# Performance work log

Hardware: AMD Instinct MI355X
Metric: run time of the kernel (lower is better)

The kernel has to match this reference:

```python
import jax, jax.numpy as jnp
import numpy as np

B, C, H, W = 32, 512, 28, 28
NC, NM, K = 50, 4, 5          # num_classes, num_mixtures, num_clutter_models
OCC = 0.3                     # occ_likely[0]


def setup_inputs() -> dict:
    key = jax.random.key(0)
    k1, k2, k3 = jax.random.split(key, 3)
    x = jax.random.uniform(k1, (B, C, H, W), dtype=jnp.float32)
    mix_model = jax.random.uniform(k2, (NC * NM, C, H, W), dtype=jnp.float32)
    clutter_model = jax.random.uniform(k3, (K, C), dtype=jnp.float32)
    return {"x": x, "mix_model": mix_model, "clutter_model": clutter_model}


def _l1_normalize(a, axis):
    # torch: F.normalize(torch.clamp(a, 0, 1), p=1, dim=axis) with eps=1e-12
    a = jnp.clip(a, 0.0, 1.0)
    return a / jnp.maximum(jnp.sum(a, axis=axis, keepdims=True), 1e-12)


def reference(x, mix_model, clutter_model):
    # clutter: [K, C] -> L1-normalized over channels
    cl = _l1_normalize(clutter_model, axis=1)
    # background log-likelihood: (x.unsqueeze(1) * cl[:, :, None, None]).sum(2)
    bg = jnp.einsum('bchw,kc->bkhw', x, cl)            # [B, K, H, W]
    bg = jnp.log(bg * OCC + 1e-10)
    # mixture models: [M, C, H, W] -> L1-normalized over channels
    mm = _l1_normalize(mix_model, axis=1)
    # foreground log-likelihood: (x.unsqueeze(1) * mm).sum(2)
    fg = jnp.einsum('bchw,mchw->bmhw', x, mm)          # [B, M, H, W]
    fg = jnp.log(fg * (1.0 - OCC) + 1e-10)
    fg = fg.reshape(B, NC, NM, 1, H, W)
    # per-pixel occlusion max between foreground and background, sum over H, W
    per_model = jnp.maximum(fg, bg[:, None, None, :, :, :]).sum((-1, -2))  # [B, NC, NM, K]
    # max over clutter models, then over mixtures
    return per_model.max(axis=-1).max(axis=-1)          # [B, NC]
```

## Files before the change

kernel.cpp:

```cpp
#include <hip/hip_runtime.h>
#include <math.h>

#define Bc  32
#define Cc  512
#define HWc 784
#define Mc  200
#define Kc  5
#define NCc 50

#define PTm   16
#define MTm   16
#define NMB   13
#define NPB   49
#define CKm   32
#define NCHm  16
#define RSTR  18
#define XPL   (32*RSTR)
#define MPL   (16*RSTR)
#define MMBASE (16*XPL)
#define LDSDW (16*XPL + 16*MPL)

typedef short s8v __attribute__((ext_vector_type(8)));
typedef float f4v __attribute__((ext_vector_type(4)));

union F8 { uint2 u2[2]; s8v h; };

__device__ __forceinline__ unsigned f2b(float f) {
    union { float f; unsigned u; } v; v.f = f;
    return (v.u + 0x7FFFu + ((v.u >> 16) & 1u)) >> 16;
}
__device__ __forceinline__ unsigned pk(float lo, float hi) {
    return f2b(lo) | (f2b(hi) << 16);
}

__global__ __launch_bounds__(256) void k_bg(const float* __restrict__ x,
                                            const float* __restrict__ clut,
                                            float* __restrict__ bgpart) {
    __shared__ float cl[Kc * Cc];
    __shared__ float csum[Kc];
    const int t = threadIdx.x;
    for (int i = t; i < Kc * Cc; i += 256) cl[i] = clut[i];
    __syncthreads();
    if (t < 160) {
        const int k = t >> 5, l = t & 31;
        float s = 0.0f;
        for (int c = l; c < Cc; c += 32) s += cl[k * Cc + c];
#pragma unroll
        for (int off = 16; off > 0; off >>= 1) s += __shfl_down(s, off, 32);
        if (l == 0) csum[k] = fmaxf(s, 1e-12f);
    }
    __syncthreads();

    const int b = blockIdx.x;
    const int z = blockIdx.z;
    const int hw = blockIdx.y * 256 + t;
    if (hw < HWc) {
        float acc[Kc] = {0.f, 0.f, 0.f, 0.f, 0.f};
        const int cbase = z * 128;
        const float* xb = x + ((size_t)b * Cc + cbase) * HWc + hw;
#pragma unroll 4
        for (int c = 0; c < 128; ++c) {
            const float xv = xb[c * HWc];
#pragma unroll
            for (int k = 0; k < Kc; ++k) acc[k] = fmaf(xv, cl[k * Cc + cbase + c], acc[k]);
        }
#pragma unroll
        for (int k = 0; k < Kc; ++k)
            bgpart[(((z * Bc + b) * Kc) + k) * HWc + hw] = acc[k] / csum[k];
    }
}

__global__ void k_bgsum(const float* __restrict__ bgpart, float* __restrict__ bgl) {
    const int i = blockIdx.x * 256 + threadIdx.x;
    const int N = Bc * Kc * HWc;
    if (i < N) {
        const float s = bgpart[i] + bgpart[i + N] + bgpart[i + 2 * N] + bgpart[i + 3 * N];
        bgl[i] = logf(0.3f * s + 1e-10f);
    }
}

__global__ __launch_bounds__(256) __attribute__((amdgpu_waves_per_eu(2, 2)))
void k_fg(const float* __restrict__ x, const float* __restrict__ mm,
          float* __restrict__ fg) {
    __shared__ unsigned lds[LDSDW];

    const int t = threadIdx.x;
    const int mblk = blockIdx.x % NMB;
    const int pix0 = (blockIdx.x / NMB) * PTm;

    int xoff[4], xl[4];
#pragma unroll
    for (int g = 0; g < 4; ++g) {
        const int G = t + 256 * g;
        const int q = G & 3, b = (G >> 2) & 31, cg = G >> 7;
        xoff[g] = (b * Cc + cg * 4) * HWc + pix0 + 4 * q;
        xl[g]   = 4 * q * XPL + b * RSTR + cg * 2;
    }
    int moff[2], ml[2];
    float mzero[2];
#pragma unroll
    for (int g = 0; g < 2; ++g) {
        const int G = t + 256 * g;
        const int q = G & 3, mr = (G >> 2) & 15, cg = (G >> 6) & 7;
        const int mrow = mblk * MTm + mr;
        mzero[g] = (mrow < Mc) ? 1.0f : 0.0f;
        const int mc = (mrow < Mc) ? mrow : (Mc - 1);
        moff[g] = (mc * Cc + cg * 4) * HWc + pix0 + 4 * q;
        ml[g]   = MMBASE + 4 * q * MPL + mr * RSTR + cg * 2;
    }

    const int lane = t & 63;
    const int w    = t >> 6;
    const int row18q = (lane & 15) * RSTR + (lane >> 4) * 4;

    f4v accD[4][2], accS[4];
#pragma unroll
    for (int p = 0; p < 4; ++p) {
        accS[p] = (f4v)0.0f;
#pragma unroll
        for (int bt = 0; bt < 2; ++bt) accD[p][bt] = (f4v)0.0f;
    }
    const s8v ones = {0x3F80, 0x3F80, 0x3F80, 0x3F80, 0x3F80, 0x3F80, 0x3F80, 0x3F80};

#pragma unroll 1
    for (int ch = 0; ch < NCHm; ++ch) {
        __syncthreads();
        float4 LX[4][4], LM[2][4];
#pragma unroll
        for (int g = 0; g < 4; ++g)
#pragma unroll
            for (int cc = 0; cc < 4; ++cc)
                LX[g][cc] = *(const float4*)(x + xoff[g] + cc * HWc);
#pragma unroll
        for (int g = 0; g < 2; ++g)
#pragma unroll
            for (int cc = 0; cc < 4; ++cc)
                LM[g][cc] = *(const float4*)(mm + moff[g] + cc * HWc);
#pragma unroll
        for (int g = 0; g < 4; ++g) xoff[g] += CKm * HWc;
#pragma unroll
        for (int g = 0; g < 2; ++g) moff[g] += CKm * HWc;

#pragma unroll
        for (int g = 0; g < 4; ++g) {
            const float* f0 = (const float*)&LX[g][0];
            const float* f1 = (const float*)&LX[g][1];
            const float* f2 = (const float*)&LX[g][2];
            const float* f3 = (const float*)&LX[g][3];
#pragma unroll
            for (int p = 0; p < 4; ++p)
                *(uint2*)&lds[xl[g] + p * XPL] =
                    make_uint2(pk(f0[p], f1[p]), pk(f2[p], f3[p]));
        }
#pragma unroll
        for (int g = 0; g < 2; ++g) {
            const float z = mzero[g];
            const float* f0 = (const float*)&LM[g][0];
            const float* f1 = (const float*)&LM[g][1];
            const float* f2 = (const float*)&LM[g][2];
            const float* f3 = (const float*)&LM[g][3];
#pragma unroll
            for (int p = 0; p < 4; ++p)
                *(uint2*)&lds[ml[g] + p * MPL] =
                    make_uint2(pk(f0[p] * z, f1[p] * z), pk(f2[p] * z, f3[p] * z));
        }
        __syncthreads();

#pragma unroll
        for (int p = 0; p < 4; ++p) {
            const int pixg = w * 4 + p;
            const unsigned* Xp = &lds[pixg * XPL + row18q];
            const unsigned* Mp = &lds[MMBASE + pixg * MPL + row18q];
            F8 a0, a1, bf;
            a0.u2[0] = *(const uint2*)(Xp);
            a0.u2[1] = *(const uint2*)(Xp + 2);
            a1.u2[0] = *(const uint2*)(Xp + 16 * RSTR);
            a1.u2[1] = *(const uint2*)(Xp + 16 * RSTR + 2);
            bf.u2[0] = *(const uint2*)(Mp);
            bf.u2[1] = *(const uint2*)(Mp + 2);
            accD[p][0] = __builtin_amdgcn_mfma_f32_16x16x32_bf16(a0.h, bf.h, accD[p][0], 0, 0, 0);
            accD[p][1] = __builtin_amdgcn_mfma_f32_16x16x32_bf16(a1.h, bf.h, accD[p][1], 0, 0, 0);
            accS[p]    = __builtin_amdgcn_mfma_f32_16x16x32_bf16(ones, bf.h, accS[p],    0, 0, 0);
        }
    }

    const int m = mblk * MTm + (lane & 15);
    if (m < Mc) {
        const int quad = lane >> 4;
#pragma unroll
        for (int p = 0; p < 4; ++p) {
            const int hw = pix0 + w * 4 + p;
            const float scale = 0.7f / fmaxf(accS[p][0], 1e-12f);
#pragma unroll
            for (int bt = 0; bt < 2; ++bt)
#pragma unroll
                for (int r = 0; r < 4; ++r) {
                    const int b = bt * 16 + quad * 4 + r;
                    fg[((size_t)m * Bc + b) * HWc + hw] =
                        logf(accD[p][bt][r] * scale + 1e-10f);
                }
        }
    }
}

__global__ __launch_bounds__(256) void k_red(const float* __restrict__ fg,
                                             const float* __restrict__ bgl,
                                             float* __restrict__ pm) {
    const int bm = blockIdx.x;
    const int b = bm / Mc;
    const int m = bm % Mc;
    const int t = threadIdx.x;
    const float* fgp = fg + ((size_t)m * Bc + b) * HWc;
    const float* bgb = bgl + (size_t)b * Kc * HWc;

    float s[Kc] = {0.f, 0.f, 0.f, 0.f, 0.f};
    for (int hw = t; hw < HWc; hw += 256) {
        const float f = fgp[hw];
#pragma unroll
        for (int k = 0; k < Kc; ++k) s[k] += fmaxf(f, bgb[k * HWc + hw]);
    }
#pragma unroll
    for (int off = 32; off > 0; off >>= 1) {
#pragma unroll
        for (int k = 0; k < Kc; ++k) s[k] += __shfl_down(s[k], off, 64);
    }
    __shared__ float red[4][Kc];
    const int wv = t >> 6, ln = t & 63;
    if (ln == 0) {
#pragma unroll
        for (int k = 0; k < Kc; ++k) red[wv][k] = s[k];
    }
    __syncthreads();
    if (t == 0) {
        float best = -INFINITY;
#pragma unroll
        for (int k = 0; k < Kc; ++k)
            best = fmaxf(best, red[0][k] + red[1][k] + red[2][k] + red[3][k]);
        pm[bm] = best;
    }
}

__global__ void k_out(const float* __restrict__ pm, float* __restrict__ out) {
    const int i = blockIdx.x * 256 + threadIdx.x;
    if (i < Bc * NCc) {
        const int b = i / NCc, nc = i % NCc;
        const float* p = pm + (size_t)b * Mc + nc * 4;
        out[i] = fmaxf(fmaxf(p[0], p[1]), fmaxf(p[2], p[3]));
    }
}

extern "C" void kernel_launch(void* const* d_in, const int* in_sizes, int n_in,
                              void* d_out, int out_size, void* d_ws, size_t ws_size,
                              hipStream_t stream) {
    const float* x    = (const float*)d_in[0];
    const float* mixm = (const float*)d_in[1];
    const float* clut = (const float*)d_in[2];
    float* out = (float*)d_out;

    float* fg     = (float*)d_ws;
    float* bgpart = fg + (size_t)Mc * Bc * HWc;
    float* bgl    = bgpart + (size_t)4 * Bc * Kc * HWc;
    float* pm     = bgl + (size_t)Bc * Kc * HWc;

    k_bg   <<<dim3(Bc, 4, 4), 256, 0, stream>>>(x, clut, bgpart);
    k_bgsum<<<dim3((Bc * Kc * HWc + 255) / 256), 256, 0, stream>>>(bgpart, bgl);
    k_fg   <<<dim3(NMB * NPB), 256, 0, stream>>>(x, mixm, fg);
    k_red  <<<dim3(Bc * Mc), 256, 0, stream>>>(fg, bgl, pm);
    k_out  <<<dim3(7), 256, 0, stream>>>(pm, out);
}
```

Baseline: 577.5 us.

## Prefetch next channel chunk into registers and remap blocks across XCDs

The global loads for the next channel chunk are now issued right after the current chunk is written to LDS, so their latency overlaps the MFMA compute of the current chunk. Block IDs are also remapped so that consecutive logical workgroups land on the same XCD, which should improve L2 reuse of shared x and mixture-model tiles. The cost is higher register pressure from keeping the prefetch buffers live across the compute phase, under a fixed waves-per-EU setting.

```diff
diff --git a/kernel.cpp b/kernel.cpp
--- a/kernel.cpp
+++ b/kernel.cpp
@@ -85,28 +85,33 @@
     __shared__ unsigned lds[LDSDW];
 
     const int t = threadIdx.x;
-    const int mblk = blockIdx.x % NMB;
-    const int pix0 = (blockIdx.x / NMB) * PTm;
+
+    const int nwg = NMB * NPB;
+    const int q = nwg >> 3, r = nwg & 7;
+    const int xcd = blockIdx.x & 7, sidx = blockIdx.x >> 3;
+    const int wgid = (xcd < r ? xcd * (q + 1) : r * (q + 1) + (xcd - r) * q) + sidx;
+    const int mblk = wgid % NMB;
+    const int pix0 = (wgid / NMB) * PTm;
 
     int xoff[4], xl[4];
 #pragma unroll
     for (int g = 0; g < 4; ++g) {
         const int G = t + 256 * g;
-        const int q = G & 3, b = (G >> 2) & 31, cg = G >> 7;
-        xoff[g] = (b * Cc + cg * 4) * HWc + pix0 + 4 * q;
-        xl[g]   = 4 * q * XPL + b * RSTR + cg * 2;
+        const int qq = G & 3, b = (G >> 2) & 31, cg = G >> 7;
+        xoff[g] = (b * Cc + cg * 4) * HWc + pix0 + 4 * qq;
+        xl[g]   = 4 * qq * XPL + b * RSTR + cg * 2;
     }
     int moff[2], ml[2];
     float mzero[2];
 #pragma unroll
     for (int g = 0; g < 2; ++g) {
         const int G = t + 256 * g;
-        const int q = G & 3, mr = (G >> 2) & 15, cg = (G >> 6) & 7;
+        const int qq = G & 3, mr = (G >> 2) & 15, cg = (G >> 6) & 7;
         const int mrow = mblk * MTm + mr;
         mzero[g] = (mrow < Mc) ? 1.0f : 0.0f;
         const int mc = (mrow < Mc) ? mrow : (Mc - 1);
-        moff[g] = (mc * Cc + cg * 4) * HWc + pix0 + 4 * q;
-        ml[g]   = MMBASE + 4 * q * MPL + mr * RSTR + cg * 2;
+        moff[g] = (mc * Cc + cg * 4) * HWc + pix0 + 4 * qq;
+        ml[g]   = MMBASE + 4 * qq * MPL + mr * RSTR + cg * 2;
     }
 
     const int lane = t & 63;
@@ -122,24 +127,25 @@
     }
     const s8v ones = {0x3F80, 0x3F80, 0x3F80, 0x3F80, 0x3F80, 0x3F80, 0x3F80, 0x3F80};
 
+    float4 LX[4][4], LM[2][4];
+#pragma unroll
+    for (int g = 0; g < 4; ++g)
+#pragma unroll
+        for (int cc = 0; cc < 4; ++cc)
+            LX[g][cc] = *(const float4*)(x + xoff[g] + cc * HWc);
+#pragma unroll
+    for (int g = 0; g < 2; ++g)
+#pragma unroll
+        for (int cc = 0; cc < 4; ++cc)
+            LM[g][cc] = *(const float4*)(mm + moff[g] + cc * HWc);
+#pragma unroll
+    for (int g = 0; g < 4; ++g) xoff[g] += CKm * HWc;
+#pragma unroll
+    for (int g = 0; g < 2; ++g) moff[g] += CKm * HWc;
+
 #pragma unroll 1
     for (int ch = 0; ch < NCHm; ++ch) {
         __syncthreads();
-        float4 LX[4][4], LM[2][4];
-#pragma unroll
-        for (int g = 0; g < 4; ++g)
-#pragma unroll
-            for (int cc = 0; cc < 4; ++cc)
-                LX[g][cc] = *(const float4*)(x + xoff[g] + cc * HWc);
-#pragma unroll
-        for (int g = 0; g < 2; ++g)
-#pragma unroll
-            for (int cc = 0; cc < 4; ++cc)
-                LM[g][cc] = *(const float4*)(mm + moff[g] + cc * HWc);
-#pragma unroll
-        for (int g = 0; g < 4; ++g) xoff[g] += CKm * HWc;
-#pragma unroll
-        for (int g = 0; g < 2; ++g) moff[g] += CKm * HWc;
 
 #pragma unroll
         for (int g = 0; g < 4; ++g) {
@@ -164,6 +170,24 @@
                 *(uint2*)&lds[ml[g] + p * MPL] =
                     make_uint2(pk(f0[p] * z, f1[p] * z), pk(f2[p] * z, f3[p] * z));
         }
+
+        if (ch + 1 < NCHm) {
+#pragma unroll
+            for (int g = 0; g < 4; ++g)
+#pragma unroll
+                for (int cc = 0; cc < 4; ++cc)
+                    LX[g][cc] = *(const float4*)(x + xoff[g] + cc * HWc);
+#pragma unroll
+            for (int g = 0; g < 2; ++g)
+#pragma unroll
+                for (int cc = 0; cc < 4; ++cc)
+                    LM[g][cc] = *(const float4*)(mm + moff[g] + cc * HWc);
+#pragma unroll
+            for (int g = 0; g < 4; ++g) xoff[g] += CKm * HWc;
+#pragma unroll
+            for (int g = 0; g < 2; ++g) moff[g] += CKm * HWc;
+        }
+
         __syncthreads();
 
 #pragma unroll
```

Measured after the change: 560.6 us. 2.9% less time.
